# Kernel optimization log

Hardware: AMD Instinct MI355X
Metric: run time of the kernel (lower is better)

## Reference

```python
import jax, jax.numpy as jnp
import numpy as np
import math

EMBED = 256
HEADS = 8
HD = EMBED // HEADS  # 32
NB = 3               # n_behaviors
C = NB * NB + 1      # 10 behavior-pair classes
NUM_BUCKETS = 32
MAX_DIST = 40
EPS = 1e-12
B, L = 4, 512


def _rel_bucket(seq_len, num_buckets=NUM_BUCKETS, max_distance=MAX_DIST):
    """T5-style relative position buckets, matching RelativePositionBias._relative_position_bucket."""
    pos = jnp.arange(seq_len)
    relative_position = pos[None, :] - pos[:, None]  # k - q
    n = -relative_position
    nb = num_buckets // 2
    ret = (n < 0).astype(jnp.int32) * nb
    n = jnp.abs(n)
    max_exact = nb // 2
    is_small = n < max_exact
    nf = jnp.maximum(n, 1).astype(jnp.float32)  # clamp to avoid log(0); masked by is_small anyway
    val_large = max_exact + (jnp.log(nf / max_exact) / math.log(max_distance / max_exact) * (nb - max_exact)).astype(jnp.int32)
    val_large = jnp.minimum(val_large, nb - 1)
    return ret + jnp.where(is_small, n, val_large)


def setup_inputs() -> dict:
    key = jax.random.key(0)
    ks = jax.random.split(key, 12)
    s = 0.02
    return {
        "input_tensor": jax.random.normal(ks[0], (B, L, EMBED), jnp.float32),
        "attention_mask": jnp.zeros((B, 1, L, L), jnp.float32),
        "type_seq": jax.random.randint(ks[1], (B, L), 0, NB + 1),
        "Wq": jax.random.normal(ks[2], (NB + 1, EMBED, HEADS, HD), jnp.float32) * s,
        "Wk": jax.random.normal(ks[3], (NB + 1, EMBED, HEADS, HD), jnp.float32) * s,
        "Wv": jax.random.normal(ks[4], (NB + 1, EMBED, HEADS, HD), jnp.float32) * s,
        "W1": jax.random.normal(ks[5], (NB, HEADS, HD, HD), jnp.float32) * s,
        "alpha1": jax.random.normal(ks[6], (C, NB, HEADS), jnp.float32),
        "W2": jax.random.normal(ks[7], (NB, HEADS, HD, HD), jnp.float32) * s,
        "alpha2": jax.random.normal(ks[8], (C, NB, HEADS), jnp.float32),
        "rp_tables": jax.random.normal(ks[9], (C, NUM_BUCKETS, HEADS), jnp.float32) * s,
        "ln_gamma": jnp.ones((EMBED,), jnp.float32),
        "ln_beta": jnp.zeros((EMBED,), jnp.float32),
    }


def reference(input_tensor, attention_mask, type_seq, Wq, Wk, Wv, W1, alpha1, W2, alpha2, rp_tables, ln_gamma, ln_beta):
    bsz, seq_len, emb = input_tensor.shape
    ts = type_seq
    # behavior pair matrix: 0 if either side is padding, else (tq-1)*NB + tk in [1, NB^2]
    bm = ((ts[:, :, None] * ts[:, None, :]) != 0).astype(jnp.int32)
    bm = bm * ((ts[:, :, None] - 1) * NB + ts[:, None, :])  # [B,L,L]

    # --- relative position bias, gathered per behavior pair ---
    bucket = _rel_bucket(seq_len)                 # [L,L]
    vals = rp_tables[:, bucket, :]                # [C,L,L,H]
    qi = jnp.arange(seq_len)[None, :, None]
    ki = jnp.arange(seq_len)[None, None, :]
    bias = vals[bm, qi, ki]                       # [B,L,L,H] gathered along C per pair
    bias = jnp.transpose(bias, (0, 3, 1, 2))      # [B,H,L,L]

    # --- behavior-gated QKV ---
    oh = jax.nn.one_hot(ts, NB + 1, dtype=input_tensor.dtype)  # [B,L,NB+1]
    q = jnp.einsum('BLH,bHhd,BLb->BhLd', input_tensor, Wq, oh)
    k = jnp.einsum('BLH,bHhd,BLb->BhLd', input_tensor, Wk, oh)
    v = jnp.einsum('BLH,bHhd,BLb->BhLd', input_tensor, Wv, oh)

    # --- bilinear scores with per-pair mixing matrices ---
    W1_ = jnp.einsum('bhmn,Cbh->Chmn', W1, jax.nn.softmax(alpha1, axis=1))
    att_all = jnp.einsum('BhQm,Chmn,BhKn->BhQKC', q, W1_, k)  # [B,H,L,L,C]
    scores = jnp.take_along_axis(att_all, bm[:, None, :, :, None], axis=4)[..., 0]
    scores = scores * (1.0 / math.sqrt(HD)) + bias + attention_mask
    probs = jax.nn.softmax(scores, axis=-1)  # dropout=0.0 -> identity

    # --- behavior-mixed value aggregation ---
    W2_ = jnp.einsum('bhmn,Cbh->Chmn', W2, jax.nn.softmax(alpha2, axis=1))
    oh_bm = jax.nn.one_hot(bm, C, dtype=probs.dtype)          # [B,L,L,C]
    pC = probs[:, :, :, :, None] * oh_bm[:, None]             # [B,H,L,L,C]
    ctx = jnp.einsum('BhQKC,Chnm,BhKn->BhQm', pC, W2_, v)     # [B,H,L,d]

    ctx = jnp.transpose(ctx, (0, 2, 1, 3)).reshape(bsz, seq_len, emb)
    x = ctx + input_tensor  # out_dropout=0.0
    mu = jnp.mean(x, axis=-1, keepdims=True)
    var = jnp.mean(jnp.square(x - mu), axis=-1, keepdims=True)
    return (x - mu) / jnp.sqrt(var + EPS) * ln_gamma + ln_beta
```

## Files before the change

### kernel.cpp

```cpp
#include <hip/hip_runtime.h>
#include <math.h>

#define BB 4
#define LL 512
#define EMB 256
#define NH 8
#define HD 32
#define NB_ 3
#define CCN 10
#define NBKT 32
#define SCALE 0.17677669529663687f

typedef __bf16 bf16_t;
typedef __attribute__((ext_vector_type(8))) bf16_t bf16x8;
typedef __attribute__((ext_vector_type(4))) float f32x4;

__device__ __forceinline__ unsigned short f2b(float f) {
    unsigned int u = __float_as_uint(f);
    u += 0x7FFF + ((u >> 16) & 1);
    return (unsigned short)(u >> 16);
}
__device__ __forceinline__ float b2f(unsigned short s) {
    return __uint_as_float(((unsigned int)s) << 16);
}
__device__ __forceinline__ unsigned pack2(float a, float b) {
    return (unsigned)f2b(a) | ((unsigned)f2b(b) << 16);
}
__device__ __forceinline__ int bm_of(int tq, int tk) {
    return (tq * tk != 0) ? ((tq - 1) * 3 + tk) : 0;
}
__device__ __forceinline__ unsigned long long shfl_up64(unsigned long long v, int d) {
    unsigned lo = (unsigned)__shfl_up((int)(unsigned)v, d, 64);
    unsigned hi = (unsigned)__shfl_up((int)(v >> 32), d, 64);
    return (((unsigned long long)hi) << 32) | lo;
}

__device__ __forceinline__ void sort512(const int* __restrict__ tsb, int* spk,
                                        unsigned long long* wtll, int* msc, int tid) {
    int ty0 = tsb[2 * tid], ty1 = tsb[2 * tid + 1];
    unsigned long long pk = (1ULL << (16 * ty0)) + (1ULL << (16 * ty1));
    unsigned long long v = pk;
    int lane = tid & 63;
#pragma unroll
    for (int off = 1; off < 64; off <<= 1) {
        unsigned long long o = shfl_up64(v, off);
        if (lane >= off) v += o;
    }
    int w = tid >> 6;
    if (lane == 63) wtll[w] = v;
    __syncthreads();
    unsigned long long pre = 0, tot = 0;
#pragma unroll
    for (int i = 0; i < 4; i++) {
        unsigned long long xx = wtll[i];
        if (i < w) pre += xx;
        tot += xx;
    }
    v += pre;
    unsigned long long excl = v - pk;
    int c0 = (int)(tot & 0xFFFF), c1 = (int)((tot >> 16) & 0xFFFF);
    int c2 = (int)((tot >> 32) & 0xFFFF), c3 = (int)((tot >> 48) & 0xFFFF);
    int ub0 = 0, ub1 = c0, ub2 = c0 + c1, ub3 = c0 + c1 + c2;
    if (tid == 0) {
        int pc0 = (c0 + 31) & ~31, pc1 = (c1 + 31) & ~31, pc2 = (c2 + 31) & ~31, pc3 = (c3 + 31) & ~31;
        int pb1 = pc0, pb2 = pc0 + pc1, pb3 = pc0 + pc1 + pc2;
        msc[0] = 0;  msc[1] = pb1; msc[2] = pb2; msc[3] = pb3;
        msc[4] = ub0; msc[5] = ub1; msc[6] = ub2; msc[7] = ub3;
        msc[8] = c0; msc[9] = c1; msc[10] = c2; msc[11] = c3;
        msc[12] = (pb3 + pc3 + 63) & ~63;
    }
    int bases[4] = {ub0, ub1, ub2, ub3};
    int r0 = (int)((excl >> (16 * ty0)) & 0xFFFF);
    unsigned long long excl1 = excl + (1ULL << (16 * ty0));
    int r1 = (int)((excl1 >> (16 * ty1)) & 0xFFFF);
    spk[bases[ty0] + r0] = (ty0 << 16) | (2 * tid);
    spk[bases[ty1] + r1] = (ty1 << 16) | (2 * tid + 1);
    __syncthreads();
}

__device__ __forceinline__ void pad_lookup(const int* msc, int pos, int& real, int& upos, int& seg) {
    seg = (pos >= msc[1]) + (pos >= msc[2]) + (pos >= msc[3]);
    int r = pos - msc[seg];
    real = (r < msc[8 + seg]) ? 1 : 0;
    upos = msc[4 + seg] + r;
}

__global__ void k_pre(const float* __restrict__ Wq, const float* __restrict__ Wk, const float* __restrict__ Wv,
                      const int* __restrict__ ts, unsigned short* __restrict__ Wt,
                      int* __restrict__ spkg, int* __restrict__ mscg, int* __restrict__ kpadg,
                      short* __restrict__ tblg, int* __restrict__ cntg) {
    __shared__ unsigned short ls[64 * 264];
    __shared__ int spk_s[LL];
    __shared__ unsigned long long wtll[4];
    __shared__ int msc_s[16];
    int g = blockIdx.x, tid = threadIdx.x;
    if (g < 48) {
        int t = g;
        int tw = t >> 2, ob = t & 3;
        int which = tw >> 2, ty = tw & 3;
        const float* src = ((which == 0) ? Wq : (which == 1) ? Wk : Wv) + (size_t)ty * EMB * EMB;
        int out0 = ob * 64;
        for (int it = 0; it < 16; it++) {
            int e = it * 16 + (tid >> 4);
            int o4 = (tid & 15) * 4;
            float4 v = *(const float4*)&src[(size_t)e * EMB + out0 + o4];
            ls[(o4 + 0) * 264 + e] = f2b(v.x);
            ls[(o4 + 1) * 264 + e] = f2b(v.y);
            ls[(o4 + 2) * 264 + e] = f2b(v.z);
            ls[(o4 + 3) * 264 + e] = f2b(v.w);
        }
        __syncthreads();
        int out = tid >> 2, ech = (tid & 3) * 8;
        unsigned short* dst = Wt + (size_t)tw * EMB * EMB + (size_t)(out0 + out) * EMB;
        const unsigned short* srcl = &ls[out * 264];
#pragma unroll
        for (int jj = 0; jj < 8; jj++)
            *(uint4*)&dst[ech + jj * 32] = *(const uint4*)&srcl[ech + jj * 32];
        return;
    }
    if (g == 48) {
        for (int d = tid; d < LL; d += 256) {
            int v;
            if (d < 8) v = d;
            else {
                double r = log((double)d / 8.0) / log(5.0);
                v = 8 + (int)(r * 8.0);
                if (v > 15) v = 15;
            }
            tblg[d] = (short)v;
        }
        if (tid == 0) cntg[128] = 0;
        return;
    }
    {
        int b = g - 49;
        sort512(ts + b * LL, spk_s, wtll, msc_s, tid);
        for (int i = tid; i < LL; i += 256) spkg[b * LL + i] = spk_s[i];
        if (tid < 16) mscg[b * 16 + tid] = msc_s[tid];
        int KT = msc_s[12];
        for (int pos = tid; pos < KT; pos += 256) {
            int real, upos, seg;
            pad_lookup(msc_s, pos, real, upos, seg);
            int orig = real ? (spk_s[upos] & 0xFFFF) : 0x3FF;
            kpadg[b * 640 + pos] = (seg << 20) | ((real ? upos : 0) << 10) | orig;
        }
    }
}

__global__ __launch_bounds__(256, 4) void k_qkv(
    const float* __restrict__ x, const int* __restrict__ spkg, const int* __restrict__ mscg,
    const unsigned short* __restrict__ Wt,
    const float* __restrict__ A1, const float* __restrict__ W1,
    const float* __restrict__ A2, const float* __restrict__ W2,
    const float* __restrict__ am,
    float* __restrict__ W1s, float* __restrict__ W2s,
    unsigned short* __restrict__ W1Tb, unsigned short* __restrict__ W2Tb,
    int* __restrict__ cntg,
    unsigned short* __restrict__ qp, unsigned short* __restrict__ kp,
    unsigned short* __restrict__ vpT) {
    __shared__ int spk[LL];
    __shared__ int msc[16];
    __shared__ __align__(16) unsigned short vt_l[128 * 33];

    int g = blockIdx.x, tid = threadIdx.x;

    if (g >= 384) {
        int gg = g - 384;
        if (gg < 160) {
            float* cmbf = (float*)vt_l;
            int idx = gg;
            const float* alpha = (idx < 80) ? A1 : A2;
            const float* W     = (idx < 80) ? W1 : W2;
            float* Ws          = (idx < 80) ? W1s : W2s;
            unsigned short* WT = (idx < 80) ? W1Tb : W2Tb;
            idx %= 80;
            int cc = idx / NH, h = idx % NH;
            float a0 = alpha[cc * NB_ * NH + 0 * NH + h];
            float a1 = alpha[cc * NB_ * NH + 1 * NH + h];
            float a2 = alpha[cc * NB_ * NH + 2 * NH + h];
            float mx = fmaxf(a0, fmaxf(a1, a2));
            float e0 = __expf(a0 - mx), e1 = __expf(a1 - mx), e2 = __expf(a2 - mx);
            float inv = 1.0f / (e0 + e1 + e2);
            e0 *= inv; e1 *= inv; e2 *= inv;
            for (int i = tid; i < HD * HD; i += 256) {
                int m = i >> 5, n = i & 31;
                float acc = e0 * W[((0 * NH + h) * HD + m) * HD + n]
                          + e1 * W[((1 * NH + h) * HD + m) * HD + n]
                          + e2 * W[((2 * NH + h) * HD + m) * HD + n];
                cmbf[m * 33 + n] = acc;
            }
            __syncthreads();
            for (int i = tid; i < HD * HD; i += 256) {
                int a = i >> 5, bq = i & 31;
                Ws[((cc * NH + h) * HD + a) * HD + bq] = cmbf[a * 33 + bq];
                WT[((size_t)(cc * NH + h) * HD + a) * HD + bq] = f2b(cmbf[bq * 33 + a]);
            }
        } else {
            int idx = gg - 160;
            const uint4* p = (const uint4*)am + (size_t)idx * 1024;
            unsigned o = 0;
#pragma unroll
            for (int j = 0; j < 4; j++) {
                uint4 v = p[tid + j * 256];
                o |= v.x | v.y | v.z | v.w;
            }
            int wv = __any(o != 0);
            if ((tid & 63) == 0 && wv) atomicOr(&cntg[128], 1);
        }
        return;
    }

    int ns = g % 6, gb = g / 6;
    int b = gb >> 4, tb = gb & 15, i0 = tb * 32;
    int which = ns >> 1, nh = ns & 1;
    int wave = tid >> 6, lane = tid & 63, quad = lane >> 4, col = lane & 15;

    spk[tid] = spkg[b * LL + tid];
    spk[tid + 256] = spkg[b * LL + tid + 256];
    if (tid < 16) msc[tid] = mscg[b * 16 + tid];
    __syncthreads();

    bf16x8 afr[2][8];
#pragma unroll
    for (int mt = 0; mt < 2; mt++) {
        int orig = spk[i0 + mt * 16 + col] & 0xFFFF;
        const float* xr = &x[(size_t)(b * LL + orig) * EMB];
#pragma unroll
        for (int kc = 0; kc < 8; kc++) {
            float4 v0 = *(const float4*)&xr[kc * 32 + quad * 8];
            float4 v1 = *(const float4*)&xr[kc * 32 + quad * 8 + 4];
            uint4 up;
            up.x = pack2(v0.x, v0.y); up.y = pack2(v0.z, v0.w);
            up.z = pack2(v1.x, v1.y); up.w = pack2(v1.z, v1.w);
            afr[mt][kc] = *(bf16x8*)&up;
        }
    }
    int t_start = spk[i0] >> 16, t_end = spk[i0 + 31] >> 16;
    unsigned short* outp = (which == 0) ? qp : kp;

    for (int ty = t_start; ty <= t_end; ty++) {
        f32x4 acc[2][2];
#pragma unroll
        for (int mt = 0; mt < 2; mt++)
#pragma unroll
            for (int nt = 0; nt < 2; nt++) acc[mt][nt] = (f32x4){0.f, 0.f, 0.f, 0.f};
        const unsigned short* wsrc = Wt + (size_t)(which * 4 + ty) * EMB * EMB + (size_t)(nh * 128) * EMB;
        const unsigned short* w0 = &wsrc[(size_t)((wave * 2 + 0) * 16 + col) * EMB + quad * 8];
        const unsigned short* w1 = &wsrc[(size_t)((wave * 2 + 1) * 16 + col) * EMB + quad * 8];
#pragma unroll
        for (int kc = 0; kc < 8; kc++) {
            bf16x8 b0 = *(const bf16x8*)&w0[kc * 32];
            bf16x8 b1 = *(const bf16x8*)&w1[kc * 32];
            acc[0][0] = __builtin_amdgcn_mfma_f32_16x16x32_bf16(afr[0][kc], b0, acc[0][0], 0, 0, 0);
            acc[0][1] = __builtin_amdgcn_mfma_f32_16x16x32_bf16(afr[0][kc], b1, acc[0][1], 0, 0, 0);
            acc[1][0] = __builtin_amdgcn_mfma_f32_16x16x32_bf16(afr[1][kc], b0, acc[1][0], 0, 0, 0);
            acc[1][1] = __builtin_amdgcn_mfma_f32_16x16x32_bf16(afr[1][kc], b1, acc[1][1], 0, 0, 0);
        }
        if (which < 2) {
#pragma unroll
            for (int mt = 0; mt < 2; mt++)
#pragma unroll
                for (int r = 0; r < 4; r++) {
                    int tokloc = mt * 16 + quad * 4 + r;
                    int tty = spk[i0 + tokloc] >> 16;
                    if (tty != ty) continue;
#pragma unroll
                    for (int nt = 0; nt < 2; nt++) {
                        int n = nh * 128 + (wave * 2 + nt) * 16 + col;
                        int h = n >> 5, d = n & 31;
                        outp[((size_t)(b * NH + h) * LL + i0 + tokloc) * HD + d] = f2b(acc[mt][nt][r]);
                    }
                }
        } else {
#pragma unroll
            for (int mt = 0; mt < 2; mt++)
#pragma unroll
                for (int nt = 0; nt < 2; nt++) {
                    int ln = (wave * 2 + nt) * 16 + col;
#pragma unroll
                    for (int r = 0; r < 4; r++)
                        vt_l[ln * 33 + mt * 16 + quad * 4 + r] = f2b(acc[mt][nt][r]);
                }
            __syncthreads();
            int ub = msc[4 + ty], cnt = msc[8 + ty], pb = msc[ty];
            int lo = ub - i0; if (lo < 0) lo = 0;
            int hi = ub + cnt - i0; if (hi > 32) hi = 32;
            int run = hi - lo;
            int pbase = pb + i0 + lo - ub;
            int rowbase = b * 256 + nh * 128;
            int t32 = tid & 31;
            if (t32 < run) {
                for (int rr = tid >> 5; rr < 128; rr += 8)
                    vpT[(size_t)(rowbase + rr) * 640 + pbase + t32] = vt_l[rr * 33 + lo + t32];
            }
            __syncthreads();
        }
    }
}

#define SCP 648
#define OFF_UN   20736
#define OFF_QTB  29184
#define OFF_KPAD 33536
#define OFF_TBL  36096
#define OFF_RPL  37120
#define OFF_QOR  38400
#define OFF_QTY  38464
#define OFF_INV  38528
#define SM_TOTAL 38592
__global__ __launch_bounds__(256, 4) void k_attn(
    const unsigned short* __restrict__ qp, const unsigned short* __restrict__ kp,
    const unsigned short* __restrict__ vpT,
    const int* __restrict__ spkg, const int* __restrict__ mscg, const int* __restrict__ kpadg,
    const short* __restrict__ tblg,
    const float* __restrict__ rp, const float* __restrict__ am,
    const float* __restrict__ W1s, const float* __restrict__ W2s,
    const unsigned short* __restrict__ W1Tb, const unsigned short* __restrict__ W2Tb,
    const int* __restrict__ cntg, float* __restrict__ ctx) {
    __shared__ __align__(16) char smem[SM_TOTAL];
    __shared__ int msk_s;
    unsigned short* scu = (unsigned short*)smem;
    unsigned short* qstb = (unsigned short*)(smem + OFF_UN);
    float* sb   = (float*)(smem + OFF_UN);
    unsigned short* qtb = (unsigned short*)(smem + OFF_QTB);
    unsigned short* sbb = (unsigned short*)(smem + OFF_QTB);
    int*   kpad = (int*)(smem + OFF_KPAD);
    short* tbl  = (short*)(smem + OFF_TBL);
    float* rp_l = (float*)(smem + OFF_RPL);
    int*   qor_l = (int*)(smem + OFF_QOR);
    int*   qty_l = (int*)(smem + OFF_QTY);
    float* inv_l = (float*)(smem + OFF_INV);

    int blk = blockIdx.x;
    int b = blk >> 8, h = (blk >> 5) & 7, q16 = blk & 31;
    int i0q = q16 * 16;
    int tid = threadIdx.x;
    int wave = tid >> 6, lane = tid & 63, quad = lane >> 4, col = lane & 15;
    int bh = b * NH + h;

    int KT = mscg[b * 16 + 12];
    if (tid == 0) msk_s = cntg[128];
    if (tid < 16) {
        int v = spkg[b * LL + i0q + tid];
        qor_l[tid] = v & 0xFFFF; qty_l[tid] = v >> 16;
    }
    if (tid < (KT >> 2)) ((int4*)kpad)[tid] = ((const int4*)(kpadg + b * 640))[tid];
    ((int*)tbl)[tid] = ((const int*)tblg)[tid];
    for (int i = tid; i < CCN * NBKT; i += 256) rp_l[i] = rp[i * NH + h];
    {
        int q = tid >> 4, m2 = (tid & 15) * 2;
        ((unsigned*)qstb)[q * 20 + (tid & 15)] =
            *(const unsigned*)&qp[((size_t)bh * LL + i0q + q) * HD + m2];
    }
    __syncthreads();

    int qor_r[4], qty_r[4];
#pragma unroll
    for (int r = 0; r < 4; r++) { qor_r[r] = qor_l[quad * 4 + r]; qty_r[r] = qty_l[quad * 4 + r]; }
    bool uniq = (qty_l[0] == qty_l[15]);
    int tqu = qty_l[0];
    int tA = qty_l[0], tB = qty_l[15];
    bool two = false;
    if (!uniq) {
        two = true;
#pragma unroll
        for (int i = 0; i < 16; i++) {
            int t = qty_l[i];
            two = two && (t == tA || t == tB);
        }
    }
    int mz = (msk_s == 0);

    if (uniq) {
#pragma unroll
        for (int it = 0; it < 2; it++) {
            int t8 = wave * 2 + it;
            int tk = t8 >> 1, nhf = t8 & 1;
            int bmv = bm_of(tqu, tk);
            bf16x8 a = *(const bf16x8*)&qstb[col * 40 + quad * 8];
            bf16x8 bb = *(const bf16x8*)&W1Tb[((size_t)(bmv * NH + h) * HD + nhf * 16 + col) * HD + quad * 8];
            f32x4 d = {0.f, 0.f, 0.f, 0.f};
            d = __builtin_amdgcn_mfma_f32_16x16x32_bf16(a, bb, d, 0, 0, 0);
#pragma unroll
            for (int r = 0; r < 4; r++)
                qtb[(quad * 4 + r) * 136 + tk * 32 + nhf * 16 + col] = f2b(d[r]);
        }
    } else if (two) {
#pragma unroll
        for (int it = 0; it < 2; it++) {
            int t8 = wave * 2 + it;
            int tk = t8 >> 1, nhf = t8 & 1;
            bf16x8 a = *(const bf16x8*)&qstb[col * 40 + quad * 8];
            bf16x8 bA = *(const bf16x8*)&W1Tb[((size_t)(bm_of(tA, tk) * NH + h) * HD + nhf * 16 + col) * HD + quad * 8];
            bf16x8 bBv = *(const bf16x8*)&W1Tb[((size_t)(bm_of(tB, tk) * NH + h) * HD + nhf * 16 + col) * HD + quad * 8];
            f32x4 dA = {0.f, 0.f, 0.f, 0.f};
            f32x4 dB = {0.f, 0.f, 0.f, 0.f};
            dA = __builtin_amdgcn_mfma_f32_16x16x32_bf16(a, bA, dA, 0, 0, 0);
            dB = __builtin_amdgcn_mfma_f32_16x16x32_bf16(a, bBv, dB, 0, 0, 0);
#pragma unroll
            for (int r = 0; r < 4; r++) {
                float val = (qty_r[r] == tA) ? dA[r] : dB[r];
                qtb[(quad * 4 + r) * 136 + tk * 32 + nhf * 16 + col] = f2b(val);
            }
        }
    } else {
        for (int i = tid; i < 16 * 128; i += 256) {
            int q = i >> 7, r = i & 127, tk = r >> 5, n = r & 31;
            int bmv = bm_of(qty_l[q], tk);
            const float* wb = &W1s[((bmv * NH + h) * HD) * HD + n];
            float acc = 0.f;
#pragma unroll
            for (int m = 0; m < HD; m++) acc += b2f(qstb[q * 40 + m]) * wb[m * HD];
            qtb[q * 136 + tk * 32 + n] = f2b(acc);
        }
    }
    __syncthreads();

    const float* amb = am + (size_t)b * LL * LL;
    int ntiles = KT >> 4;
    for (int tile = wave; tile < ntiles; tile += 4) {
        int kb = tile * 16;
        int kv0 = kpad[kb];
        if ((kv0 & 0x3FF) == 0x3FF) {
#pragma unroll
            for (int r = 0; r < 4; r++) scu[(quad * 4 + r) * SCP + kb + col] = 0xFF80;
            continue;
        }
        int tkt = kv0 >> 20;
        int kpi = kb + col;
        int kv = kpad[kpi];
        int ko = kv & 0x3FF;
        int upos = (kv >> 10) & 0x3FF;
        bool real = (ko != 0x3FF);
        bf16x8 bfr;
        if (real) bfr = *(const bf16x8*)&kp[((size_t)bh * LL + upos) * HD + quad * 8];
        else { uint4 z = make_uint4(0, 0, 0, 0); bfr = *(bf16x8*)&z; }
        bf16x8 a = *(const bf16x8*)&qtb[col * 136 + tkt * 32 + quad * 8];
        f32x4 d = {0.f, 0.f, 0.f, 0.f};
        d = __builtin_amdgcn_mfma_f32_16x16x32_bf16(a, bfr, d, 0, 0, 0);
        if (!real) {
#pragma unroll
            for (int r = 0; r < 4; r++) scu[(quad * 4 + r) * SCP + kpi] = 0xFF80;
        } else {
#pragma unroll
            for (int r = 0; r < 4; r++) {
                int q = quad * 4 + r;
                int qo = qor_r[r];
                int dd = qo - ko;
                int ad = dd < 0 ? -dd : dd;
                int bk = (dd < 0 ? 16 : 0) + (int)tbl[ad];
                float sv = d[r] * SCALE + rp_l[bm_of(qty_r[r], tkt) * NBKT + bk];
                if (!mz) sv += amb[(size_t)qo * LL + ko];
                scu[q * SCP + kpi] = f2b(sv);
            }
        }
    }
    __syncthreads();

    {
        int gq = tid >> 4, t16 = tid & 15;
        float mx = -1e30f;
        for (int kk = t16; kk < KT; kk += 16) mx = fmaxf(mx, b2f(scu[gq * SCP + kk]));
#pragma unroll
        for (int off = 1; off < 16; off <<= 1) mx = fmaxf(mx, __shfl_xor(mx, off, 16));
        float sum = 0.f;
        for (int kk = t16; kk < KT; kk += 16) {
            int idx = gq * SCP + kk;
            float e = __expf(b2f(scu[idx]) - mx);
            scu[idx] = f2b(e); sum += e;
        }
#pragma unroll
        for (int off = 1; off < 16; off <<= 1) sum += __shfl_xor(sum, off, 16);
        if (t16 == 0) inv_l[gq] = 1.0f / sum;
    }
    __syncthreads();

    const unsigned short* vbase = &vpT[(size_t)(b * 256 + h * 32) * 640];
    f32x4 accv[2];
    accv[0] = (f32x4){0.f, 0.f, 0.f, 0.f};
    accv[1] = (f32x4){0.f, 0.f, 0.f, 0.f};
    {
        int pb = mscg[b * 16 + wave];
        int cnt = mscg[b * 16 + 8 + wave];
        int g0 = pb >> 5, g1 = (pb + cnt + 31) >> 5;
        for (int gg = g0; gg < g1; ++gg) {
            int loc = gg << 5;
            bf16x8 a = *(const bf16x8*)&scu[col * SCP + loc + quad * 8];
            bf16x8 b0 = *(const bf16x8*)&vbase[(size_t)col * 640 + loc + quad * 8];
            bf16x8 b1 = *(const bf16x8*)&vbase[(size_t)(col + 16) * 640 + loc + quad * 8];
            accv[0] = __builtin_amdgcn_mfma_f32_16x16x32_bf16(a, b0, accv[0], 0, 0, 0);
            accv[1] = __builtin_amdgcn_mfma_f32_16x16x32_bf16(a, b1, accv[1], 0, 0, 0);
        }
    }
#pragma unroll
    for (int hh = 0; hh < 2; hh++)
#pragma unroll
        for (int r = 0; r < 4; r++) {
            int q = quad * 4 + r, n = col + 16 * hh;
            float fin = accv[hh][r];
            sb[q * 132 + wave * 32 + n] = fin;
            sbb[q * 136 + wave * 32 + n] = f2b(fin);
        }
    __syncthreads();

    if (uniq) {
        if (wave < 2) {
            int mhf = wave;
            f32x4 d = {0.f, 0.f, 0.f, 0.f};
#pragma unroll
            for (int tk = 0; tk < 4; tk++) {
                int bmv = bm_of(tqu, tk);
                bf16x8 a = *(const bf16x8*)&sbb[col * 136 + tk * 32 + quad * 8];
                bf16x8 bb = *(const bf16x8*)&W2Tb[((size_t)(bmv * NH + h) * HD + mhf * 16 + col) * HD + quad * 8];
                d = __builtin_amdgcn_mfma_f32_16x16x32_bf16(a, bb, d, 0, 0, 0);
            }
#pragma unroll
            for (int r = 0; r < 4; r++) {
                int q = quad * 4 + r;
                ctx[((size_t)(b * LL + qor_l[q])) * EMB + h * HD + mhf * 16 + col] = d[r] * inv_l[q];
            }
        }
    } else if (two) {
        int myT = (wave < 2) ? tA : tB;
        int mhf = wave & 1;
        f32x4 d = {0.f, 0.f, 0.f, 0.f};
#pragma unroll
        for (int tk = 0; tk < 4; tk++) {
            int bmv = bm_of(myT, tk);
            bf16x8 a = *(const bf16x8*)&sbb[col * 136 + tk * 32 + quad * 8];
            bf16x8 bb = *(const bf16x8*)&W2Tb[((size_t)(bmv * NH + h) * HD + mhf * 16 + col) * HD + quad * 8];
            d = __builtin_amdgcn_mfma_f32_16x16x32_bf16(a, bb, d, 0, 0, 0);
        }
#pragma unroll
        for (int r = 0; r < 4; r++) {
            int q = quad * 4 + r;
            if (qty_l[q] == myT)
                ctx[((size_t)(b * LL + qor_l[q])) * EMB + h * HD + mhf * 16 + col] = d[r] * inv_l[q];
        }
    } else {
        int m = tid & 31, qq = tid >> 5;
#pragma unroll
        for (int rep = 0; rep < 2; rep++) {
            int qi = qq + 8 * rep;
            int tq = qty_l[qi];
            float acc = 0.f;
#pragma unroll
            for (int tk2 = 0; tk2 < 4; tk2++) {
                int bmv = bm_of(tq, tk2);
                const float* wb = &W2s[((bmv * NH + h) * HD) * HD + m];
                const float* sbp = &sb[qi * 132 + tk2 * 32];
                for (int n = 0; n < HD; n++) acc += sbp[n] * wb[n * HD];
            }
            int qo = qor_l[qi];
            ctx[((size_t)(b * LL + qo)) * EMB + h * HD + m] = acc * inv_l[qi];
        }
    }
}

__global__ void k_ln(const float* __restrict__ ctx, const float* __restrict__ x,
                     const float* __restrict__ gamma, const float* __restrict__ beta,
                     float* __restrict__ out) {
    int wave = threadIdx.x >> 6, lane = threadIdx.x & 63;
    int tok = blockIdx.x * 4 + wave;
    size_t base = (size_t)tok * EMB + lane * 4;
    float4 c = *(const float4*)&ctx[base];
    float4 xi = *(const float4*)&x[base];
    float4 v;
    v.x = c.x + xi.x; v.y = c.y + xi.y; v.z = c.z + xi.z; v.w = c.w + xi.w;
    float s = v.x + v.y + v.z + v.w;
    float s2 = v.x * v.x + v.y * v.y + v.z * v.z + v.w * v.w;
#pragma unroll
    for (int off = 1; off < 64; off <<= 1) {
        s += __shfl_xor(s, off, 64);
        s2 += __shfl_xor(s2, off, 64);
    }
    float mu = s * (1.0f / EMB);
    float var = s2 * (1.0f / EMB) - mu * mu;
    float r = rsqrtf(var + 1e-12f);
    float4 gg = *(const float4*)&gamma[lane * 4];
    float4 bb = *(const float4*)&beta[lane * 4];
    float4 o;
    o.x = (v.x - mu) * r * gg.x + bb.x;
    o.y = (v.y - mu) * r * gg.y + bb.y;
    o.z = (v.z - mu) * r * gg.z + bb.z;
    o.w = (v.w - mu) * r * gg.w + bb.w;
    *(float4*)&out[base] = o;
}

extern "C" void kernel_launch(void* const* d_in, const int* in_sizes, int n_in,
                              void* d_out, int out_size, void* d_ws, size_t ws_size,
                              hipStream_t stream) {
    const float* x  = (const float*)d_in[0];
    const float* am = (const float*)d_in[1];
    const int*   ts = (const int*)d_in[2];
    const float* Wq = (const float*)d_in[3];
    const float* Wk = (const float*)d_in[4];
    const float* Wv = (const float*)d_in[5];
    const float* W1 = (const float*)d_in[6];
    const float* a1 = (const float*)d_in[7];
    const float* W2 = (const float*)d_in[8];
    const float* a2 = (const float*)d_in[9];
    const float* rp = (const float*)d_in[10];
    const float* g  = (const float*)d_in[11];
    const float* be = (const float*)d_in[12];
    float* out = (float*)d_out;

    float* ws  = (float*)d_ws;
    float* W1s = ws;
    float* W2s = ws + 81920;
    unsigned short* W1Tb = (unsigned short*)(ws + 163840);
    unsigned short* W2Tb = (unsigned short*)(ws + 204800);
    int* cntg = (int*)(ws + 245760);
    int* spkg = (int*)(ws + 246016);
    int* mscg = (int*)(ws + 248064);
    int* kpadg = (int*)(ws + 248128);
    short* tblg = (short*)(ws + 250688);
    unsigned short* qp = (unsigned short*)(ws + 250944);
    unsigned short* kp = qp + BB * NH * LL * HD;
    unsigned short* vpT = kp + BB * NH * LL * HD;
    float* ctx = (float*)(vpT + BB * 256 * 640);
    unsigned short* Wt = (unsigned short*)ctx;

    hipLaunchKernelGGL(k_pre, dim3(53), dim3(256), 0, stream,
                       Wq, Wk, Wv, ts, Wt, spkg, mscg, kpadg, tblg, cntg);
    hipLaunchKernelGGL(k_qkv, dim3(800), dim3(256), 0, stream,
                       x, spkg, mscg, Wt, a1, W1, a2, W2, am, W1s, W2s, W1Tb, W2Tb, cntg,
                       qp, kp, vpT);
    hipLaunchKernelGGL(k_attn, dim3(BB * NH * 32), dim3(256), 0, stream,
                       qp, kp, vpT, spkg, mscg, kpadg, tblg, rp, am, W1s, W2s, W1Tb, W2Tb,
                       cntg, ctx);
    hipLaunchKernelGGL(k_ln, dim3(BB * LL / 4), dim3(256), 0, stream, ctx, x, g, be, out);
}
```

Measured before the change: 127.3 us.

## Merge preprocessing kernel into QKV projection kernel with per-block weight conversion

Removes the separate k_pre launch. Each QKV block now sorts the type sequence itself and converts its fp32 weight slice to a transposed bf16 tile in LDS, instead of reading a pre-transposed bf16 weight buffer. The global mask-detection atomic is replaced by per-block flags that the attention kernel reduces. This saves one launch and a dependency barrier, but it repeats the sort and the weight conversion in every block, adds LDS usage, and lowers launch bounds occupancy from 4 to 3.

```diff
diff --git a/kernel.cpp b/kernel.cpp
--- a/kernel.cpp
+++ b/kernel.cpp
@@ -85,89 +85,33 @@
     upos = msc[4 + seg] + r;
 }
 
-__global__ void k_pre(const float* __restrict__ Wq, const float* __restrict__ Wk, const float* __restrict__ Wv,
-                      const int* __restrict__ ts, unsigned short* __restrict__ Wt,
-                      int* __restrict__ spkg, int* __restrict__ mscg, int* __restrict__ kpadg,
-                      short* __restrict__ tblg, int* __restrict__ cntg) {
-    __shared__ unsigned short ls[64 * 264];
-    __shared__ int spk_s[LL];
-    __shared__ unsigned long long wtll[4];
-    __shared__ int msc_s[16];
-    int g = blockIdx.x, tid = threadIdx.x;
-    if (g < 48) {
-        int t = g;
-        int tw = t >> 2, ob = t & 3;
-        int which = tw >> 2, ty = tw & 3;
-        const float* src = ((which == 0) ? Wq : (which == 1) ? Wk : Wv) + (size_t)ty * EMB * EMB;
-        int out0 = ob * 64;
-        for (int it = 0; it < 16; it++) {
-            int e = it * 16 + (tid >> 4);
-            int o4 = (tid & 15) * 4;
-            float4 v = *(const float4*)&src[(size_t)e * EMB + out0 + o4];
-            ls[(o4 + 0) * 264 + e] = f2b(v.x);
-            ls[(o4 + 1) * 264 + e] = f2b(v.y);
-            ls[(o4 + 2) * 264 + e] = f2b(v.z);
-            ls[(o4 + 3) * 264 + e] = f2b(v.w);
-        }
-        __syncthreads();
-        int out = tid >> 2, ech = (tid & 3) * 8;
-        unsigned short* dst = Wt + (size_t)tw * EMB * EMB + (size_t)(out0 + out) * EMB;
-        const unsigned short* srcl = &ls[out * 264];
-#pragma unroll
-        for (int jj = 0; jj < 8; jj++)
-            *(uint4*)&dst[ech + jj * 32] = *(const uint4*)&srcl[ech + jj * 32];
-        return;
-    }
-    if (g == 48) {
-        for (int d = tid; d < LL; d += 256) {
-            int v;
-            if (d < 8) v = d;
-            else {
-                double r = log((double)d / 8.0) / log(5.0);
-                v = 8 + (int)(r * 8.0);
-                if (v > 15) v = 15;
-            }
-            tblg[d] = (short)v;
-        }
-        if (tid == 0) cntg[128] = 0;
-        return;
-    }
-    {
-        int b = g - 49;
-        sort512(ts + b * LL, spk_s, wtll, msc_s, tid);
-        for (int i = tid; i < LL; i += 256) spkg[b * LL + i] = spk_s[i];
-        if (tid < 16) mscg[b * 16 + tid] = msc_s[tid];
-        int KT = msc_s[12];
-        for (int pos = tid; pos < KT; pos += 256) {
-            int real, upos, seg;
-            pad_lookup(msc_s, pos, real, upos, seg);
-            int orig = real ? (spk_s[upos] & 0xFFFF) : 0x3FF;
-            kpadg[b * 640 + pos] = (seg << 20) | ((real ? upos : 0) << 10) | orig;
-        }
-    }
-}
-
-__global__ __launch_bounds__(256, 4) void k_qkv(
-    const float* __restrict__ x, const int* __restrict__ spkg, const int* __restrict__ mscg,
-    const unsigned short* __restrict__ Wt,
+__global__ __launch_bounds__(256, 3) void k_main(
+    const float* __restrict__ x, const int* __restrict__ ts,
+    const float* __restrict__ Wq, const float* __restrict__ Wk, const float* __restrict__ Wv,
     const float* __restrict__ A1, const float* __restrict__ W1,
     const float* __restrict__ A2, const float* __restrict__ W2,
     const float* __restrict__ am,
     float* __restrict__ W1s, float* __restrict__ W2s,
     unsigned short* __restrict__ W1Tb, unsigned short* __restrict__ W2Tb,
-    int* __restrict__ cntg,
+    int* __restrict__ mfl,
+    int* __restrict__ spkg, int* __restrict__ mscg, int* __restrict__ kpadg,
+    short* __restrict__ tblg,
     unsigned short* __restrict__ qp, unsigned short* __restrict__ kp,
     unsigned short* __restrict__ vpT) {
-    __shared__ int spk[LL];
-    __shared__ int msc[16];
-    __shared__ __align__(16) unsigned short vt_l[128 * 33];
+    __shared__ __align__(16) char sm1[44384];
+    int* spk_s = (int*)sm1;
+    unsigned long long* wtll = (unsigned long long*)(sm1 + 2048);
+    int* msc_s = (int*)(sm1 + 2080);
+    unsigned short* vt_l = (unsigned short*)(sm1 + 2144);
+    unsigned short* wlds = (unsigned short*)(sm1 + 10592);
+    float* cmbf = (float*)(sm1 + 10592);
+    int* reds = (int*)(sm1 + 2048);
 
     int g = blockIdx.x, tid = threadIdx.x;
 
     if (g >= 384) {
         int gg = g - 384;
         if (gg < 160) {
-            float* cmbf = (float*)vt_l;
             int idx = gg;
             const float* alpha = (idx < 80) ? A1 : A2;
             const float* W     = (idx < 80) ? W1 : W2;
@@ -195,17 +139,46 @@
                 Ws[((cc * NH + h) * HD + a) * HD + bq] = cmbf[a * 33 + bq];
                 WT[((size_t)(cc * NH + h) * HD + a) * HD + bq] = f2b(cmbf[bq * 33 + a]);
             }
-        } else {
+            return;
+        }
+        if (gg < 288) {
             int idx = gg - 160;
-            const uint4* p = (const uint4*)am + (size_t)idx * 1024;
+            const uint4* p = (const uint4*)am + (size_t)idx * 2048;
             unsigned o = 0;
 #pragma unroll
-            for (int j = 0; j < 4; j++) {
+            for (int j = 0; j < 8; j++) {
                 uint4 v = p[tid + j * 256];
                 o |= v.x | v.y | v.z | v.w;
             }
             int wv = __any(o != 0);
-            if ((tid & 63) == 0 && wv) atomicOr(&cntg[128], 1);
+            if ((tid & 63) == 0) reds[tid >> 6] = wv;
+            __syncthreads();
+            if (tid == 0) mfl[idx] = reds[0] | reds[1] | reds[2] | reds[3];
+            return;
+        }
+        if (gg < 292) {
+            int b = gg - 288;
+            sort512(ts + b * LL, spk_s, wtll, msc_s, tid);
+            for (int i = tid; i < LL; i += 256) spkg[b * LL + i] = spk_s[i];
+            if (tid < 16) mscg[b * 16 + tid] = msc_s[tid];
+            int KT = msc_s[12];
+            for (int pos = tid; pos < KT; pos += 256) {
+                int real, upos, seg;
+                pad_lookup(msc_s, pos, real, upos, seg);
+                int orig = real ? (spk_s[upos] & 0xFFFF) : 0x3FF;
+                kpadg[b * 640 + pos] = (seg << 20) | ((real ? upos : 0) << 10) | orig;
+            }
+            return;
+        }
+        for (int d = tid; d < LL; d += 256) {
+            int v;
+            if (d < 8) v = d;
+            else {
+                double r = log((double)d / 8.0) / log(5.0);
+                v = 8 + (int)(r * 8.0);
+                if (v > 15) v = 15;
+            }
+            tblg[d] = (short)v;
         }
         return;
     }
@@ -215,15 +188,12 @@
     int which = ns >> 1, nh = ns & 1;
     int wave = tid >> 6, lane = tid & 63, quad = lane >> 4, col = lane & 15;
 
-    spk[tid] = spkg[b * LL + tid];
-    spk[tid + 256] = spkg[b * LL + tid + 256];
-    if (tid < 16) msc[tid] = mscg[b * 16 + tid];
-    __syncthreads();
+    sort512(ts + b * LL, spk_s, wtll, msc_s, tid);
 
     bf16x8 afr[2][8];
 #pragma unroll
     for (int mt = 0; mt < 2; mt++) {
-        int orig = spk[i0 + mt * 16 + col] & 0xFFFF;
+        int orig = spk_s[i0 + mt * 16 + col] & 0xFFFF;
         const float* xr = &x[(size_t)(b * LL + orig) * EMB];
 #pragma unroll
         for (int kc = 0; kc < 8; kc++) {
@@ -235,54 +205,66 @@
             afr[mt][kc] = *(bf16x8*)&up;
         }
     }
-    int t_start = spk[i0] >> 16, t_end = spk[i0 + 31] >> 16;
+    int ttyv[2][4];
+#pragma unroll
+    for (int mt = 0; mt < 2; mt++)
+#pragma unroll
+        for (int r = 0; r < 4; r++)
+            ttyv[mt][r] = spk_s[i0 + mt * 16 + quad * 4 + r] >> 16;
+
+    int t_start = spk_s[i0] >> 16, t_end = spk_s[i0 + 31] >> 16;
     unsigned short* outp = (which == 0) ? qp : kp;
+    const float* wmat = (which == 0) ? Wq : (which == 1) ? Wk : Wv;
 
     for (int ty = t_start; ty <= t_end; ty++) {
-        f32x4 acc[2][2];
-#pragma unroll
-        for (int mt = 0; mt < 2; mt++)
-#pragma unroll
-            for (int nt = 0; nt < 2; nt++) acc[mt][nt] = (f32x4){0.f, 0.f, 0.f, 0.f};
-        const unsigned short* wsrc = Wt + (size_t)(which * 4 + ty) * EMB * EMB + (size_t)(nh * 128) * EMB;
-        const unsigned short* w0 = &wsrc[(size_t)((wave * 2 + 0) * 16 + col) * EMB + quad * 8];
-        const unsigned short* w1 = &wsrc[(size_t)((wave * 2 + 1) * 16 + col) * EMB + quad * 8];
-#pragma unroll
-        for (int kc = 0; kc < 8; kc++) {
-            bf16x8 b0 = *(const bf16x8*)&w0[kc * 32];
-            bf16x8 b1 = *(const bf16x8*)&w1[kc * 32];
-            acc[0][0] = __builtin_amdgcn_mfma_f32_16x16x32_bf16(afr[0][kc], b0, acc[0][0], 0, 0, 0);
-            acc[0][1] = __builtin_amdgcn_mfma_f32_16x16x32_bf16(afr[0][kc], b1, acc[0][1], 0, 0, 0);
-            acc[1][0] = __builtin_amdgcn_mfma_f32_16x16x32_bf16(afr[1][kc], b0, acc[1][0], 0, 0, 0);
-            acc[1][1] = __builtin_amdgcn_mfma_f32_16x16x32_bf16(afr[1][kc], b1, acc[1][1], 0, 0, 0);
-        }
-        if (which < 2) {
-#pragma unroll
-            for (int mt = 0; mt < 2; mt++)
-#pragma unroll
-                for (int r = 0; r < 4; r++) {
-                    int tokloc = mt * 16 + quad * 4 + r;
-                    int tty = spk[i0 + tokloc] >> 16;
-                    if (tty != ty) continue;
-#pragma unroll
-                    for (int nt = 0; nt < 2; nt++) {
-                        int n = nh * 128 + (wave * 2 + nt) * 16 + col;
+        const float* wty = wmat + (size_t)ty * EMB * EMB;
+#pragma unroll
+        for (int half = 0; half < 2; half++) {
+            int n0 = nh * 128 + half * 64;
+            __syncthreads();
+            for (int it = 0; it < 16; it++) {
+                int k = it * 16 + (tid >> 4);
+                int nl = (tid & 15) * 4;
+                float4 v = *(const float4*)&wty[(size_t)k * EMB + n0 + nl];
+                wlds[(nl + 0) * 264 + k] = f2b(v.x);
+                wlds[(nl + 1) * 264 + k] = f2b(v.y);
+                wlds[(nl + 2) * 264 + k] = f2b(v.z);
+                wlds[(nl + 3) * 264 + k] = f2b(v.w);
+            }
+            __syncthreads();
+            f32x4 acc[2];
+            acc[0] = (f32x4){0.f, 0.f, 0.f, 0.f};
+            acc[1] = (f32x4){0.f, 0.f, 0.f, 0.f};
+            const unsigned short* wrow = &wlds[(wave * 16 + col) * 264 + quad * 8];
+#pragma unroll
+            for (int kc = 0; kc < 8; kc++) {
+                bf16x8 bb = *(const bf16x8*)&wrow[kc * 32];
+                acc[0] = __builtin_amdgcn_mfma_f32_16x16x32_bf16(afr[0][kc], bb, acc[0], 0, 0, 0);
+                acc[1] = __builtin_amdgcn_mfma_f32_16x16x32_bf16(afr[1][kc], bb, acc[1], 0, 0, 0);
+            }
+            if (which < 2) {
+#pragma unroll
+                for (int mt = 0; mt < 2; mt++)
+#pragma unroll
+                    for (int r = 0; r < 4; r++) {
+                        if (ttyv[mt][r] != ty) continue;
+                        int tokloc = mt * 16 + quad * 4 + r;
+                        int n = n0 + wave * 16 + col;
                         int h = n >> 5, d = n & 31;
-                        outp[((size_t)(b * NH + h) * LL + i0 + tokloc) * HD + d] = f2b(acc[mt][nt][r]);
+                        outp[((size_t)(b * NH + h) * LL + i0 + tokloc) * HD + d] = f2b(acc[mt][r]);
                     }
-                }
-        } else {
-#pragma unroll
-            for (int mt = 0; mt < 2; mt++)
-#pragma unroll
-                for (int nt = 0; nt < 2; nt++) {
-                    int ln = (wave * 2 + nt) * 16 + col;
+            } else {
+                int ln = half * 64 + wave * 16 + col;
+#pragma unroll
+                for (int mt = 0; mt < 2; mt++)
 #pragma unroll
                     for (int r = 0; r < 4; r++)
-                        vt_l[ln * 33 + mt * 16 + quad * 4 + r] = f2b(acc[mt][nt][r]);
-                }
+                        vt_l[ln * 33 + mt * 16 + quad * 4 + r] = f2b(acc[mt][r]);
+            }
+        }
+        if (which == 2) {
             __syncthreads();
-            int ub = msc[4 + ty], cnt = msc[8 + ty], pb = msc[ty];
+            int ub = msc_s[4 + ty], cnt = msc_s[8 + ty], pb = msc_s[ty];
             int lo = ub - i0; if (lo < 0) lo = 0;
             int hi = ub + cnt - i0; if (hi > 32) hi = 32;
             int run = hi - lo;
@@ -316,7 +298,7 @@
     const float* __restrict__ rp, const float* __restrict__ am,
     const float* __restrict__ W1s, const float* __restrict__ W2s,
     const unsigned short* __restrict__ W1Tb, const unsigned short* __restrict__ W2Tb,
-    const int* __restrict__ cntg, float* __restrict__ ctx) {
+    const int* __restrict__ mfl, float* __restrict__ ctx) {
     __shared__ __align__(16) char smem[SM_TOTAL];
     __shared__ int msk_s;
     unsigned short* scu = (unsigned short*)smem;
@@ -339,7 +321,11 @@
     int bh = b * NH + h;
 
     int KT = mscg[b * 16 + 12];
-    if (tid == 0) msk_s = cntg[128];
+    if (wave == 0) {
+        int v = mfl[lane] | mfl[64 + lane];
+        int anyv = __any(v != 0);
+        if (lane == 0) msk_s = anyv;
+    }
     if (tid < 16) {
         int v = spkg[b * LL + i0q + tid];
         qor_l[tid] = v & 0xFFFF; qty_l[tid] = v >> 16;
@@ -610,7 +596,7 @@
     float* W2s = ws + 81920;
     unsigned short* W1Tb = (unsigned short*)(ws + 163840);
     unsigned short* W2Tb = (unsigned short*)(ws + 204800);
-    int* cntg = (int*)(ws + 245760);
+    int* mfl  = (int*)(ws + 245760);
     int* spkg = (int*)(ws + 246016);
     int* mscg = (int*)(ws + 248064);
     int* kpadg = (int*)(ws + 248128);
@@ -619,15 +605,13 @@
     unsigned short* kp = qp + BB * NH * LL * HD;
     unsigned short* vpT = kp + BB * NH * LL * HD;
     float* ctx = (float*)(vpT + BB * 256 * 640);
-    unsigned short* Wt = (unsigned short*)ctx;
-
-    hipLaunchKernelGGL(k_pre, dim3(53), dim3(256), 0, stream,
-                       Wq, Wk, Wv, ts, Wt, spkg, mscg, kpadg, tblg, cntg);
-    hipLaunchKernelGGL(k_qkv, dim3(800), dim3(256), 0, stream,
-                       x, spkg, mscg, Wt, a1, W1, a2, W2, am, W1s, W2s, W1Tb, W2Tb, cntg,
+
+    hipLaunchKernelGGL(k_main, dim3(677), dim3(256), 0, stream,
+                       x, ts, Wq, Wk, Wv, a1, W1, a2, W2, am,
+                       W1s, W2s, W1Tb, W2Tb, mfl, spkg, mscg, kpadg, tblg,
                        qp, kp, vpT);
     hipLaunchKernelGGL(k_attn, dim3(BB * NH * 32), dim3(256), 0, stream,
                        qp, kp, vpT, spkg, mscg, kpadg, tblg, rp, am, W1s, W2s, W1Tb, W2Tb,
-                       cntg, ctx);
+                       mfl, ctx);
     hipLaunchKernelGGL(k_ln, dim3(BB * LL / 4), dim3(256), 0, stream, ctx, x, g, be, out);
 }
```

Result: slower. 133.4 us (+4.8%).
